# Optimization experiments

Hardware: AMD Instinct MI355X
Metric: run time of the kernel (lower is better)

## Reference

```python
import jax, jax.numpy as jnp
import numpy as np

EPS = 1e-5  # instance-norm epsilon (NormalizeLayer over spatial axes)

def instance_norm(x):
    # normalize over spatial axes (1,2) per sample, per channel
    mean = jnp.mean(x, axis=(1, 2), keepdims=True)
    var = jnp.var(x, axis=(1, 2), keepdims=True)
    return (x - mean) / jnp.sqrt(var + EPS)

def l2norm(x, axis=-1):
    return x / jnp.sqrt(jnp.sum(x * x, axis=axis, keepdims=True) + 1e-12)

def setup_inputs() -> dict:
    key = jax.random.key(0)
    ks = jax.random.split(key, 5)
    B, H, W, C = 4, 64, 64, 256
    content = jax.random.normal(ks[0], (B, H, W, C), jnp.float32)
    style = jax.random.normal(ks[1], (B, H, W, C), jnp.float32)
    scale = 1.0 / np.sqrt(C)
    Wq = jax.random.normal(ks[2], (C, C), jnp.float32) * scale
    Wk = jax.random.normal(ks[3], (C, C), jnp.float32) * scale
    Wv = jax.random.normal(ks[4], (C, C), jnp.float32) * scale
    bq = jnp.zeros((C,), jnp.float32)
    bk = jnp.zeros((C,), jnp.float32)
    bv = jnp.zeros((C,), jnp.float32)
    return {"content": content, "style": style, "Wq": Wq, "bq": bq,
            "Wk": Wk, "bk": bk, "Wv": Wv, "bv": bv}

def reference(content, style, Wq, bq, Wk, bk, Wv, bv):
    B, H, W, C = content.shape
    N = H * W
    norm_content = instance_norm(content)
    norm_style = instance_norm(style)
    # 1x1 convs == per-pixel linear layers
    Q = (jnp.einsum('bhwc,cd->bhwd', norm_content, Wq) + bq).reshape(B, N, C)
    K = (jnp.einsum('bhwc,cd->bhwd', norm_style, Wk) + bk).reshape(B, N, C)
    V = (jnp.einsum('bhwc,cd->bhwd', style, Wv) + bv).reshape(B, N, C)
    # cosine-similarity attention (Dot with normalize=True)
    attn = jnp.einsum('bnc,bmc->bnm', l2norm(Q), l2norm(K))  # [B, N, N]
    A = jax.nn.softmax(attn, axis=-1)
    M = jnp.einsum('bnm,bmc->bnc', A, V)                 # weighted mean
    S2 = jnp.einsum('bnm,bmc->bnc', A, V * V) - M * M    # weighted variance
    S2 = jax.nn.relu(S2)
    # safe sqrt: grad-safe at exactly 0 (matches sqrt(relu(x)) values)
    S = jnp.where(S2 > 0, jnp.sqrt(jnp.where(S2 > 0, S2, 1.0)), 0.0)
    S = S.reshape(B, H, W, C)
    M = M.reshape(B, H, W, C)
    return S * norm_content + M
```

## Files before the change

### kernel.cpp

```cpp
#include <hip/hip_runtime.h>
#include <cstdint>

#define BB 4
#define NN 4096
#define CC 256

typedef __attribute__((ext_vector_type(8))) short bf16x8;
typedef __attribute__((ext_vector_type(4))) short bf16x4;
typedef __attribute__((ext_vector_type(4))) float f32x4;
typedef unsigned int u32;
typedef __attribute__((ext_vector_type(4))) u32 u32x4;

#define MFMA_BF16(a, b, c) __builtin_amdgcn_mfma_f32_16x16x32_bf16((a), (b), (c), 0, 0, 0)
#define MFMA_FP8(a, b, c)  __builtin_amdgcn_mfma_f32_16x16x32_fp8_fp8((a), (b), (c), 0, 0, 0)

#define WAITCNT(vm, xp, lgkm) (((vm) & 0xF) | (((vm) >> 4) << 14) | ((xp) << 4) | ((lgkm) << 8))

__device__ __forceinline__ unsigned short f2bf(float f) {
  union { float f; unsigned u; } v; v.f = f;
  unsigned r = v.u + 0x7fffu + ((v.u >> 16) & 1u);
  return (unsigned short)(r >> 16);
}
__device__ __forceinline__ float bf2f(unsigned short h) {
  union { unsigned u; float f; } v; v.u = ((unsigned)h) << 16;
  return v.f;
}
__device__ __forceinline__ u32 pk4_fp8(float a, float b, float c, float d) {
  u32 v = (u32)__builtin_amdgcn_cvt_pk_fp8_f32(a, b, 0, false);
  v = (u32)__builtin_amdgcn_cvt_pk_fp8_f32(c, d, (int)v, true);
  return v;
}

typedef __attribute__((address_space(3))) unsigned int lds_u32;
typedef __attribute__((address_space(1))) unsigned int glb_u32;

__device__ __forceinline__ void async_cp16(const void* g, void* l) {
  __builtin_amdgcn_global_load_lds((const glb_u32*)g,
                                   (lds_u32*)(unsigned)(unsigned long long)l,
                                   16, 0, 0);
}

__global__ __launch_bounds__(256) void transpose_w(const float* __restrict__ Wq,
                                                   const float* __restrict__ Wk,
                                                   const float* __restrict__ Wv,
                                                   unsigned short* __restrict__ Wt) {
  __shared__ float sT[64 * 65];
  int blk = blockIdx.x;
  int z = blk / 16, tl = blk % 16;
  int c0 = (tl >> 2) * 64, d0 = (tl & 3) * 64;
  const float* W = (z == 0) ? Wq : ((z == 1) ? Wk : Wv);
  #pragma unroll
  for (int i = 0; i < 16; ++i) {
    int e = i * 256 + threadIdx.x;
    int c = e >> 6, d = e & 63;
    sT[c * 65 + d] = W[(size_t)(c0 + c) * CC + d0 + d];
  }
  __syncthreads();
  #pragma unroll
  for (int i = 0; i < 16; ++i) {
    int e = i * 256 + threadIdx.x;
    int d = e >> 6, c = e & 63;
    Wt[(size_t)z * 65536 + (size_t)(d0 + d) * CC + c0 + c] = f2bf(sT[c * 65 + d]);
  }
}

__global__ __launch_bounds__(256) void stats_partial(const float* __restrict__ content,
                                                     const float* __restrict__ style,
                                                     float* __restrict__ sums) {
  int blk = blockIdx.x;
  int t = blk >> 9, b = (blk >> 7) & 3, chunk = blk & 127;
  const float* X = t ? style : content;
  int c = threadIdx.x;
  const float* base = X + ((size_t)b * NN + (size_t)chunk * 32) * CC + c;
  float s = 0.f, ss = 0.f;
  #pragma unroll 8
  for (int r = 0; r < 32; ++r) {
    float x = base[(size_t)r * CC];
    s += x; ss += x * x;
  }
  atomicAdd(&sums[((t * 2 + 0) * BB + b) * CC + c], s);
  atomicAdd(&sums[((t * 2 + 1) * BB + b) * CC + c], ss);
}

__global__ __launch_bounds__(256) void stats_finalize(const float* __restrict__ sums,
                                                      float* __restrict__ stats) {
  int i = blockIdx.x * 256 + threadIdx.x;
  int t = i >> 10, bc = i & 1023;
  float s = sums[(t * 2 + 0) * 1024 + bc];
  float ss = sums[(t * 2 + 1) * 1024 + bc];
  float m = s * (1.0f / NN);
  float var = ss * (1.0f / NN) - m * m;
  stats[(t * 2 + 0) * 1024 + bc] = m;
  stats[(t * 2 + 1) * 1024 + bc] = rsqrtf(var + 1e-5f);
}

__global__ __launch_bounds__(256, 2) void qkv_kernel(
    const float* __restrict__ content, const float* __restrict__ style,
    const unsigned short* __restrict__ Wt,
    const float* __restrict__ bq, const float* __restrict__ bk, const float* __restrict__ bv,
    const float* __restrict__ stats,
    unsigned char* __restrict__ Qn, unsigned char* __restrict__ Kn,
    unsigned char* __restrict__ Vct) {
  __shared__ unsigned short sX[64 * 256];
  __shared__ unsigned short sWOT[256 * 64];
  __shared__ float sSq[64];

  int tid = threadIdx.x;
  int wid = tid >> 6, lane = tid & 63, quad = lane >> 4, l16 = lane & 15;
  int uwid = __builtin_amdgcn_readfirstlane(wid);
  int tileid = blockIdx.x;
  int z = blockIdx.y;
  int gr0 = tileid * 64;
  int b = gr0 >> 12;

  const float* X = (z == 0) ? content : style;
  int statt = (z == 0) ? 0 : 1;
  const float* mean = stats + ((statt * 2 + 0) * BB + b) * CC;
  const float* rstd = stats + ((statt * 2 + 1) * BB + b) * CC;
  bool donorm = (z < 2);

  if (tid < 64) sSq[tid] = 0.f;

  {
    int row = tid >> 2;
    int c0 = (tid & 3) * 64;
    const float* xr = X + (size_t)(gr0 + row) * CC;
    #pragma unroll
    for (int i = 0; i < 8; ++i) {
      int c = c0 + i * 8;
      f32x4 xa = *(const f32x4*)(xr + c);
      f32x4 xb = *(const f32x4*)(xr + c + 4);
      float xv[8] = {xa.x, xa.y, xa.z, xa.w, xb.x, xb.y, xb.z, xb.w};
      bf16x8 hh;
      #pragma unroll
      for (int j = 0; j < 8; ++j) {
        float x = xv[j];
        if (donorm) x = (x - mean[c + j]) * rstd[c + j];
        hh[j] = (short)f2bf(x);
      }
      int jchunk = (tid & 3) * 8 + (i ^ (row & 7));
      *(bf16x8*)(sX + row * 256 + jchunk * 8) = hh;
    }
  }

  f32x4 zero4 = {0.f, 0.f, 0.f, 0.f};
  f32x4 acc[4][4];
  #pragma unroll
  for (int i = 0; i < 4; ++i)
    #pragma unroll
    for (int j = 0; j < 4; ++j) acc[i][j] = zero4;

  int n0 = wid * 64;
  const unsigned short* wb = Wt + (size_t)z * 65536;

  for (int chn = 0; chn < 4; ++chn) {
    int kk0 = chn * 64;
    __syncthreads();
    #pragma unroll
    for (int it = 0; it < 8; ++it) {
      int L = it * 256 + wid * 64 + lane;
      int d = L >> 3, s = L & 7;
      int j = s ^ (d & 7);
      async_cp16(wb + d * 256 + kk0 + j * 8,
                 (char*)sWOT + (size_t)(it * 256 + uwid * 64) * 16);
    }
    __syncthreads();
    #pragma unroll
    for (int ks = 0; ks < 2; ++ks) {
      bf16x8 a[4];
      #pragma unroll
      for (int mf = 0; mf < 4; ++mf) {
        int row = mf * 16 + l16;
        int j = chn * 8 + ((ks * 4 + quad) ^ (row & 7));
        a[mf] = *(const bf16x8*)(sX + row * 256 + j * 8);
      }
      #pragma unroll
      for (int nf = 0; nf < 4; ++nf) {
        int d = n0 + nf * 16 + l16;
        int j = (ks * 4 + quad) ^ (d & 7);
        bf16x8 bw = *(const bf16x8*)(sWOT + d * 64 + j * 8);
        #pragma unroll
        for (int mf = 0; mf < 4; ++mf) acc[mf][nf] = MFMA_BF16(a[mf], bw, acc[mf][nf]);
      }
    }
  }

  const float* bias = (z == 0) ? bq : ((z == 1) ? bk : bv);
  #pragma unroll
  for (int nf = 0; nf < 4; ++nf) {
    float bb_ = bias[n0 + nf * 16 + l16];
    #pragma unroll
    for (int mf = 0; mf < 4; ++mf) {
      acc[mf][nf].x += bb_; acc[mf][nf].y += bb_;
      acc[mf][nf].z += bb_; acc[mf][nf].w += bb_;
    }
  }

  if (z < 2) {
    #pragma unroll
    for (int mf = 0; mf < 4; ++mf) {
      f32x4 ss = zero4;
      #pragma unroll
      for (int nf = 0; nf < 4; ++nf) ss += acc[mf][nf] * acc[mf][nf];
      #pragma unroll
      for (int m = 1; m < 16; m <<= 1) {
        ss.x += __shfl_xor(ss.x, m, 64);
        ss.y += __shfl_xor(ss.y, m, 64);
        ss.z += __shfl_xor(ss.z, m, 64);
        ss.w += __shfl_xor(ss.w, m, 64);
      }
      if (l16 == 0) {
        int r0 = mf * 16 + quad * 4;
        atomicAdd(&sSq[r0 + 0], ss.x);
        atomicAdd(&sSq[r0 + 1], ss.y);
        atomicAdd(&sSq[r0 + 2], ss.z);
        atomicAdd(&sSq[r0 + 3], ss.w);
      }
    }
    __syncthreads();
    if (tid < 64) sSq[tid] = rsqrtf(sSq[tid] + 1e-12f);
    __syncthreads();
    unsigned char* O = (z == 0) ? Qn : Kn;
    #pragma unroll
    for (int mf = 0; mf < 4; ++mf) {
      int r0 = mf * 16 + quad * 4;
      float rn0 = sSq[r0], rn1 = sSq[r0 + 1], rn2 = sSq[r0 + 2], rn3 = sSq[r0 + 3];
      #pragma unroll
      for (int nf = 0; nf < 4; ++nf) {
        int col = n0 + nf * 16 + l16;
        u32 p01 = (u32)__builtin_amdgcn_cvt_pk_fp8_f32(acc[mf][nf].x * rn0, acc[mf][nf].y * rn1, 0, false);
        u32 p23 = (u32)__builtin_amdgcn_cvt_pk_fp8_f32(acc[mf][nf].z * rn2, acc[mf][nf].w * rn3, 0, false);
        O[(size_t)(gr0 + r0 + 0) * CC + col] = (unsigned char)(p01 & 0xff);
        O[(size_t)(gr0 + r0 + 1) * CC + col] = (unsigned char)((p01 >> 8) & 0xff);
        O[(size_t)(gr0 + r0 + 2) * CC + col] = (unsigned char)(p23 & 0xff);
        O[(size_t)(gr0 + r0 + 3) * CC + col] = (unsigned char)((p23 >> 8) & 0xff);
      }
    }
  } else {
    __syncthreads();
    #pragma unroll
    for (int mf = 0; mf < 4; ++mf) {
      int j0 = mf * 2 + (quad >> 1);
      int sub = (quad & 1) * 4;
      #pragma unroll
      for (int nf = 0; nf < 4; ++nf) {
        int col = n0 + nf * 16 + l16;
        bf16x4 pk;
        pk[0] = (short)f2bf(acc[mf][nf].x);
        pk[1] = (short)f2bf(acc[mf][nf].y);
        pk[2] = (short)f2bf(acc[mf][nf].z);
        pk[3] = (short)f2bf(acc[mf][nf].w);
        *(bf16x4*)(sWOT + col * 64 + (j0 ^ (col & 7)) * 8 + sub) = pk;
      }
    }
    __syncthreads();
    int n_in_b = gr0 & (NN - 1);
    unsigned char* vrow  = Vct + ((size_t)(b * 512 + tid)) * NN + n_in_b;
    unsigned char* v2row = Vct + ((size_t)(b * 512 + 256 + tid)) * NN + n_in_b;
    #pragma unroll
    for (int i = 0; i < 4; ++i) {
      float f[16];
      #pragma unroll
      for (int g = 0; g < 2; ++g) {
        bf16x8 hv = *(const bf16x8*)(sWOT + tid * 64 + ((i * 2 + g) ^ (tid & 7)) * 8);
        #pragma unroll
        for (int j = 0; j < 8; ++j) f[g * 8 + j] = bf2f((unsigned short)hv[j]);
      }
      u32x4 v1, v2;
      v1.x = pk4_fp8(f[0], f[1], f[2], f[3]);
      v1.y = pk4_fp8(f[4], f[5], f[6], f[7]);
      v1.z = pk4_fp8(f[8], f[9], f[10], f[11]);
      v1.w = pk4_fp8(f[12], f[13], f[14], f[15]);
      v2.x = pk4_fp8(f[0]*f[0], f[1]*f[1], f[2]*f[2], f[3]*f[3]);
      v2.y = pk4_fp8(f[4]*f[4], f[5]*f[5], f[6]*f[6], f[7]*f[7]);
      v2.z = pk4_fp8(f[8]*f[8], f[9]*f[9], f[10]*f[10], f[11]*f[11]);
      v2.w = pk4_fp8(f[12]*f[12], f[13]*f[13], f[14]*f[14], f[15]*f[15]);
      *(u32x4*)(vrow + i * 16) = v1;
      *(u32x4*)(v2row + i * 16) = v2;
    }
  }
}

__global__ __launch_bounds__(512, 2) void flash_kernel(
    const unsigned char* __restrict__ Qn,
    const unsigned char* __restrict__ Kn,
    const unsigned char* __restrict__ Vct,
    const float* __restrict__ content,
    const float* __restrict__ stats,
    float* __restrict__ out) {
  __shared__ __align__(16) char smem[32768 + 65536 + 4096 + 256];
  char* sKb = smem;
  char* sVb = smem + 32768;
  char* sP  = smem + 98304;
  float* sL = (float*)(smem + 102400);
  float* sE2 = (float*)smem;

  int tid = threadIdx.x;
  int wid = tid >> 6, lane = tid & 63, quad = lane >> 4, l16 = lane & 15;
  int uwid = __builtin_amdgcn_readfirstlane(wid);

  int id = blockIdx.x;
  int b = (id >> 1) & 3;
  int tile = ((id >> 3) << 1) | (id & 1);
  int q0 = tile * 64;

  int qh = (wid & 1) * 32;
  int kb0 = (wid >> 1) * 16;
  int cw = wid * 64;

  long qf[2][8];
  #pragma unroll
  for (int mf = 0; mf < 2; ++mf) {
    int row = q0 + qh + mf * 16 + l16;
    const unsigned char* base = Qn + (((size_t)b * NN + row) << 8);
    #pragma unroll
    for (int kf = 0; kf < 8; ++kf)
      qf[mf][kf] = *(const long*)(base + kf * 32 + quad * 8);
  }
  __builtin_amdgcn_s_waitcnt(WAITCNT(0, 7, 15));

  if (tid < 64) sL[tid] = 0.f;

  const unsigned char* kbp = Kn + (((size_t)b * NN) << 8);
  const unsigned char* vbp = Vct + ((size_t)b * 512) * NN;

  auto stageK = [&](int k0, int buf) {
    char* dst = sKb + buf * 16384;
    #pragma unroll
    for (int it = 0; it < 2; ++it) {
      int L = it * 512 + wid * 64 + lane;
      int ky = L >> 4, s = L & 15;
      int c16 = s ^ (ky & 15);
      async_cp16(kbp + (((size_t)(k0 + ky)) << 8) + c16 * 16,
                 dst + (size_t)(it * 512 + uwid * 64) * 16);
    }
  };
  auto stageV = [&](int k0, int buf) {
    char* dst = sVb + buf * 32768;
    #pragma unroll
    for (int it = 0; it < 4; ++it) {
      int L = it * 512 + wid * 64 + lane;
      int r128 = L >> 3, s8 = L & 7;
      int x = s8 ^ (r128 & 7);
      int ch = (r128 << 1) | (x >> 2);
      int k16 = x & 3;
      async_cp16(vbp + (size_t)ch * NN + k0 + k16 * 16,
                 dst + (size_t)(it * 512 + uwid * 64) * 16);
    }
  };

  f32x4 zero4 = {0.f, 0.f, 0.f, 0.f};
  f32x4 om[4][4];
  #pragma unroll
  for (int i = 0; i < 4; ++i)
    #pragma unroll
    for (int j = 0; j < 4; ++j) om[i][j] = zero4;
  float Lr[8];
  #pragma unroll
  for (int i = 0; i < 8; ++i) Lr[i] = 0.f;

  stageK(0, 0);  stageV(0, 0);
  stageK(64, 1); stageV(64, 1);

  int keyrow = (kb0 + l16) * 256;
  int key15 = l16;
  int khalf = (quad & 1) * 8;

  for (int kt = 0; kt < 64; ++kt) {
    __builtin_amdgcn_s_waitcnt(WAITCNT(6, 7, 15));
    __builtin_amdgcn_s_barrier();

    const char* sKc = sKb + (kt & 1) * 16384;
    f32x4 s0 = zero4, s1 = zero4;
    #pragma unroll
    for (int kf = 0; kf < 8; ++kf) {
      int slot = (kf * 2 + (quad >> 1)) ^ key15;
      long bk = *(const long*)(sKc + keyrow + slot * 16 + khalf);
      s0 = MFMA_FP8(qf[0][kf], bk, s0);
      s1 = MFMA_FP8(qf[1][kf], bk, s1);
    }
    #pragma unroll
    for (int mf = 0; mf < 2; ++mf) {
      f32x4 sv = mf ? s1 : s0;
      float p0 = __expf(sv.x), p1 = __expf(sv.y), p2 = __expf(sv.z), p3 = __expf(sv.w);
      Lr[mf * 4 + 0] += p0; Lr[mf * 4 + 1] += p1;
      Lr[mf * 4 + 2] += p2; Lr[mf * 4 + 3] += p3;
      u32 b01 = (u32)__builtin_amdgcn_cvt_pk_fp8_f32(p0, p1, 0, false);
      u32 b23 = (u32)__builtin_amdgcn_cvt_pk_fp8_f32(p2, p3, 0, false);
      int qbase = qh + mf * 16 + quad * 4;
      #pragma unroll
      for (int r = 0; r < 4; ++r) {
        int q = qbase + r;
        u32 byte = (r < 2) ? ((r == 0) ? (b01 & 0xff) : ((b01 >> 8) & 0xff))
                           : ((r == 2) ? (b23 & 0xff) : ((b23 >> 8) & 0xff));
        int addr = (q >> 1) * 128 + ((((q & 1) * 4 + (wid >> 1))) ^ ((q >> 1) & 7)) * 16 + l16;
        sP[addr] = (unsigned char)byte;
      }
    }
    __builtin_amdgcn_s_waitcnt(WAITCNT(63, 7, 0));
    __builtin_amdgcn_s_barrier();

    const char* sVc = sVb + (kt & 1) * 32768;
    long pf[2][4], vf[2][4];
    #pragma unroll
    for (int ks = 0; ks < 2; ++ks) {
      int c16 = ks * 2 + (quad >> 1);
      #pragma unroll
      for (int mf2 = 0; mf2 < 4; ++mf2) {
        int q = mf2 * 16 + l16;
        pf[ks][mf2] = *(const long*)(sP + (q >> 1) * 128 +
                        (((q & 1) * 4 + c16) ^ ((q >> 1) & 7)) * 16 + khalf);
      }
      #pragma unroll
      for (int nf = 0; nf < 4; ++nf) {
        int ch = cw + nf * 16 + l16;
        vf[ks][nf] = *(const long*)(sVc + (ch >> 1) * 128 +
                        (((ch & 1) * 4 + c16) ^ ((ch >> 1) & 7)) * 16 + khalf);
      }
    }
    __builtin_amdgcn_s_waitcnt(WAITCNT(63, 7, 0));
    __builtin_amdgcn_s_barrier();

    int nk = ((kt + 2) & 63) * 64;
    stageK(nk, kt & 1);
    stageV(nk, kt & 1);

    #pragma unroll
    for (int ks = 0; ks < 2; ++ks)
      #pragma unroll
      for (int nf = 0; nf < 4; ++nf)
        #pragma unroll
        for (int mf2 = 0; mf2 < 4; ++mf2)
          om[mf2][nf] = MFMA_FP8(pf[ks][mf2], vf[ks][nf], om[mf2][nf]);
  }

  #pragma unroll
  for (int i = 0; i < 8; ++i) {
    #pragma unroll
    for (int m = 1; m < 16; m <<= 1) Lr[i] += __shfl_xor(Lr[i], m, 64);
  }
  if (l16 == 0) {
    #pragma unroll
    for (int mf = 0; mf < 2; ++mf)
      #pragma unroll
      for (int r = 0; r < 4; ++r)
        atomicAdd(&sL[qh + mf * 16 + quad * 4 + r], Lr[mf * 4 + r]);
  }
  __builtin_amdgcn_s_waitcnt(WAITCNT(0, 7, 0));
  __builtin_amdgcn_s_barrier();

  if (wid >= 4) {
    #pragma unroll
    for (int mf2 = 0; mf2 < 4; ++mf2) {
      #pragma unroll
      for (int nf = 0; nf < 4; ++nf) {
        int ch = (wid - 4) * 64 + nf * 16 + l16;
        int cidx = (mf2 * 4 + quad) ^ (ch & 15);
        *(f32x4*)(sE2 + ch * 64 + cidx * 4) = om[mf2][nf];
      }
    }
  }
  __syncthreads();

  if (wid < 4) {
    const float* meanc = stats + (0 * BB + b) * CC;
    const float* rstdc = stats + (1 * BB + b) * CC;
    float linv[4][4];
    #pragma unroll
    for (int mf2 = 0; mf2 < 4; ++mf2)
      #pragma unroll
      for (int r = 0; r < 4; ++r)
        linv[mf2][r] = 1.0f / sL[mf2 * 16 + quad * 4 + r];
    #pragma unroll
    for (int nf = 0; nf < 4; ++nf) {
      int ch = cw + nf * 16 + l16;
      float mc = meanc[ch], rc = rstdc[ch];
      #pragma unroll
      for (int mf2 = 0; mf2 < 4; ++mf2) {
        int cidx = (mf2 * 4 + quad) ^ (ch & 15);
        f32x4 vv = *(const f32x4*)(sE2 + ch * 64 + cidx * 4);
        f32x4 ov = om[mf2][nf];
        #pragma unroll
        for (int r = 0; r < 4; ++r) {
          int row = mf2 * 16 + quad * 4 + r;
          float li = linv[mf2][r];
          float ovr = (r == 0) ? ov.x : (r == 1) ? ov.y : (r == 2) ? ov.z : ov.w;
          float vvr = (r == 0) ? vv.x : (r == 1) ? vv.y : (r == 2) ? vv.z : vv.w;
          float M = ovr * li;
          float E2 = vvr * li;
          float S2 = E2 - M * M;
          float S = (S2 > 0.f) ? sqrtf(S2) : 0.f;
          size_t gi = (((size_t)b * NN + q0 + row) << 8) + ch;
          float xh = (content[gi] - mc) * rc;
          out[gi] = S * xh + M;
        }
      }
    }
  }
}

extern "C" void kernel_launch(void* const* d_in, const int* in_sizes, int n_in,
                              void* d_out, int out_size, void* d_ws, size_t ws_size,
                              hipStream_t stream) {
  const float* content = (const float*)d_in[0];
  const float* style   = (const float*)d_in[1];
  const float* Wq = (const float*)d_in[2];
  const float* bq = (const float*)d_in[3];
  const float* Wk = (const float*)d_in[4];
  const float* bk = (const float*)d_in[5];
  const float* Wv = (const float*)d_in[6];
  const float* bv = (const float*)d_in[7];
  char* ws = (char*)d_ws;

  float* sums        = (float*)(ws + 0);
  float* stats       = (float*)(ws + 16384);
  unsigned short* Wt = (unsigned short*)(ws + 32768);
  unsigned char* Qn  = (unsigned char*)(ws + 425984);
  unsigned char* Kn  = (unsigned char*)(ws + 4620288);
  unsigned char* Vct = (unsigned char*)(ws + 8814592);
  float* outp = (float*)d_out;

  hipMemsetAsync(d_ws, 0, 16384, stream);
  hipLaunchKernelGGL(transpose_w, dim3(48), dim3(256), 0, stream, Wq, Wk, Wv, Wt);
  hipLaunchKernelGGL(stats_partial, dim3(1024), dim3(256), 0, stream, content, style, sums);
  hipLaunchKernelGGL(stats_finalize, dim3(8), dim3(256), 0, stream, sums, stats);
  hipLaunchKernelGGL(qkv_kernel, dim3(256, 3), dim3(256), 0, stream,
                     content, style, Wt, bq, bk, bv, stats, Qn, Kn, Vct);
  hipLaunchKernelGGL(flash_kernel, dim3(256), dim3(512), 0, stream,
                     Qn, Kn, Vct, content, stats, outp);
}
```

Before: 249.4 us.

## Restructure flash kernel to 32-query tiles with 256-thread blocks

Halves the query tile per block (32 rows) and the block size (4 waves), doubling the grid to 512 blocks. Each wave now computes scores for its own 16-key slice with K as the A operand and writes P as packed 32-bit words into a double-buffered P tile. V is single-buffered and staged one tile ahead, with V fragments loaded before the barrier, which removes one barrier per iteration. The aim is better CU occupancy and less LDS per block, at the cost of twice the K/V traffic per query, since each block streams all keys for fewer queries.

```diff
diff --git a/kernel.cpp b/kernel.cpp
--- a/kernel.cpp
+++ b/kernel.cpp
@@ -281,18 +281,20 @@
   }
 }
 
-__global__ __launch_bounds__(512, 2) void flash_kernel(
+__global__ __launch_bounds__(256, 2) void flash_kernel(
     const unsigned char* __restrict__ Qn,
     const unsigned char* __restrict__ Kn,
     const unsigned char* __restrict__ Vct,
     const float* __restrict__ content,
     const float* __restrict__ stats,
     float* __restrict__ out) {
-  __shared__ __align__(16) char smem[32768 + 65536 + 4096 + 256];
+  __shared__ __align__(16) char smem[32768 + 32768 + 4096 + 128];
   char* sKb = smem;
-  char* sVb = smem + 32768;
-  char* sP  = smem + 98304;
-  float* sL = (float*)(smem + 102400);
+  char* sVb = smem + 65536;
+  char* sPb = smem + 32768;
+  sVb = smem + 36864;
+  sPb = smem + 32768;
+  float* sL = (float*)(smem + 69632);
   float* sE2 = (float*)smem;
 
   int tid = threadIdx.x;
@@ -302,24 +304,19 @@
   int id = blockIdx.x;
   int b = (id >> 1) & 3;
   int tile = ((id >> 3) << 1) | (id & 1);
-  int q0 = tile * 64;
-
-  int qh = (wid & 1) * 32;
-  int kb0 = (wid >> 1) * 16;
-  int cw = wid * 64;
+  int q0 = tile * 32;
 
   long qf[2][8];
   #pragma unroll
-  for (int mf = 0; mf < 2; ++mf) {
-    int row = q0 + qh + mf * 16 + l16;
-    const unsigned char* base = Qn + (((size_t)b * NN + row) << 8);
+  for (int ng = 0; ng < 2; ++ng) {
+    const unsigned char* base = Qn + (((size_t)b * NN + q0 + ng * 16 + l16) << 8);
     #pragma unroll
     for (int kf = 0; kf < 8; ++kf)
-      qf[mf][kf] = *(const long*)(base + kf * 32 + quad * 8);
+      qf[ng][kf] = *(const long*)(base + kf * 32 + quad * 8);
   }
   __builtin_amdgcn_s_waitcnt(WAITCNT(0, 7, 15));
 
-  if (tid < 64) sL[tid] = 0.f;
+  if (tid < 32) sL[tid] = 0.f;
 
   const unsigned char* kbp = Kn + (((size_t)b * NN) << 8);
   const unsigned char* vbp = Vct + ((size_t)b * 512) * NN;
@@ -327,163 +324,143 @@
   auto stageK = [&](int k0, int buf) {
     char* dst = sKb + buf * 16384;
     #pragma unroll
-    for (int it = 0; it < 2; ++it) {
-      int L = it * 512 + wid * 64 + lane;
-      int ky = L >> 4, s = L & 15;
-      int c16 = s ^ (ky & 15);
+    for (int it = 0; it < 4; ++it) {
+      int L = it * 256 + wid * 64 + lane;
+      int ky = L >> 4;
+      int c16 = (L & 15) ^ (ky & 15);
       async_cp16(kbp + (((size_t)(k0 + ky)) << 8) + c16 * 16,
-                 dst + (size_t)(it * 512 + uwid * 64) * 16);
+                 dst + (size_t)(it * 256 + uwid * 64) * 16);
     }
   };
-  auto stageV = [&](int k0, int buf) {
-    char* dst = sVb + buf * 32768;
-    #pragma unroll
-    for (int it = 0; it < 4; ++it) {
-      int L = it * 512 + wid * 64 + lane;
-      int r128 = L >> 3, s8 = L & 7;
-      int x = s8 ^ (r128 & 7);
-      int ch = (r128 << 1) | (x >> 2);
-      int k16 = x & 3;
-      async_cp16(vbp + (size_t)ch * NN + k0 + k16 * 16,
-                 dst + (size_t)(it * 512 + uwid * 64) * 16);
+  auto stageV = [&](int k0) {
+    #pragma unroll
+    for (int it = 0; it < 8; ++it) {
+      int L = it * 256 + wid * 64 + lane;
+      int ch = L >> 2;
+      int c16 = (L & 3) ^ ((ch >> 1) & 3);
+      async_cp16(vbp + (size_t)ch * NN + k0 + c16 * 16,
+                 sVb + (size_t)(it * 256 + uwid * 64) * 16);
     }
   };
 
   f32x4 zero4 = {0.f, 0.f, 0.f, 0.f};
-  f32x4 om[4][4];
-  #pragma unroll
-  for (int i = 0; i < 4; ++i)
-    #pragma unroll
-    for (int j = 0; j < 4; ++j) om[i][j] = zero4;
-  float Lr[8];
-  #pragma unroll
-  for (int i = 0; i < 8; ++i) Lr[i] = 0.f;
-
-  stageK(0, 0);  stageV(0, 0);
-  stageK(64, 1); stageV(64, 1);
-
-  int keyrow = (kb0 + l16) * 256;
-  int key15 = l16;
-  int khalf = (quad & 1) * 8;
+  f32x4 om[2][8];
+  #pragma unroll
+  for (int i = 0; i < 2; ++i)
+    #pragma unroll
+    for (int j = 0; j < 8; ++j) om[i][j] = zero4;
+  float Lr[2] = {0.f, 0.f};
+
+  stageK(0, 0);
+  stageV(0);
+  stageK(64, 1);
+
+  int cwch[2];
+  (void)cwch;
 
   for (int kt = 0; kt < 64; ++kt) {
-    __builtin_amdgcn_s_waitcnt(WAITCNT(6, 7, 15));
+    __builtin_amdgcn_s_waitcnt(WAITCNT(4, 7, 15));
     __builtin_amdgcn_s_barrier();
 
     const char* sKc = sKb + (kt & 1) * 16384;
+    char* sPc = sPb + (kt & 1) * 2048;
+
     f32x4 s0 = zero4, s1 = zero4;
     #pragma unroll
     for (int kf = 0; kf < 8; ++kf) {
-      int slot = (kf * 2 + (quad >> 1)) ^ key15;
-      long bk = *(const long*)(sKc + keyrow + slot * 16 + khalf);
-      s0 = MFMA_FP8(qf[0][kf], bk, s0);
-      s1 = MFMA_FP8(qf[1][kf], bk, s1);
-    }
-    #pragma unroll
-    for (int mf = 0; mf < 2; ++mf) {
-      f32x4 sv = mf ? s1 : s0;
+      long ak = *(const long*)(sKc + (wid * 16 + l16) * 256 +
+                               ((kf * 2 + (quad >> 1)) ^ l16) * 16 + (quad & 1) * 8);
+      s0 = MFMA_FP8(ak, qf[0][kf], s0);
+      s1 = MFMA_FP8(ak, qf[1][kf], s1);
+    }
+    #pragma unroll
+    for (int ng = 0; ng < 2; ++ng) {
+      f32x4 sv = ng ? s1 : s0;
       float p0 = __expf(sv.x), p1 = __expf(sv.y), p2 = __expf(sv.z), p3 = __expf(sv.w);
-      Lr[mf * 4 + 0] += p0; Lr[mf * 4 + 1] += p1;
-      Lr[mf * 4 + 2] += p2; Lr[mf * 4 + 3] += p3;
-      u32 b01 = (u32)__builtin_amdgcn_cvt_pk_fp8_f32(p0, p1, 0, false);
-      u32 b23 = (u32)__builtin_amdgcn_cvt_pk_fp8_f32(p2, p3, 0, false);
-      int qbase = qh + mf * 16 + quad * 4;
-      #pragma unroll
-      for (int r = 0; r < 4; ++r) {
-        int q = qbase + r;
-        u32 byte = (r < 2) ? ((r == 0) ? (b01 & 0xff) : ((b01 >> 8) & 0xff))
-                           : ((r == 2) ? (b23 & 0xff) : ((b23 >> 8) & 0xff));
-        int addr = (q >> 1) * 128 + ((((q & 1) * 4 + (wid >> 1))) ^ ((q >> 1) & 7)) * 16 + l16;
-        sP[addr] = (unsigned char)byte;
-      }
-    }
+      Lr[ng] += p0 + p1 + p2 + p3;
+      u32 w = pk4_fp8(p0, p1, p2, p3);
+      int q = ng * 16 + l16;
+      int chunk8 = wid * 2 + (quad >> 1);
+      *(u32*)(sPc + q * 64 + ((chunk8 ^ (q & 7)) * 8) + (quad & 1) * 4) = w;
+    }
+    long vf[2][8];
+    #pragma unroll
+    for (int ks = 0; ks < 2; ++ks)
+      #pragma unroll
+      for (int cg = 0; cg < 8; ++cg) {
+        int ch = wid * 128 + cg * 16 + l16;
+        int slot = (ks * 2 + (quad >> 1)) ^ ((ch >> 1) & 3);
+        vf[ks][cg] = *(const long*)(sVb + ch * 64 + slot * 16 + (quad & 1) * 8);
+      }
     __builtin_amdgcn_s_waitcnt(WAITCNT(63, 7, 0));
     __builtin_amdgcn_s_barrier();
 
-    const char* sVc = sVb + (kt & 1) * 32768;
-    long pf[2][4], vf[2][4];
-    #pragma unroll
-    for (int ks = 0; ks < 2; ++ks) {
-      int c16 = ks * 2 + (quad >> 1);
-      #pragma unroll
-      for (int mf2 = 0; mf2 < 4; ++mf2) {
-        int q = mf2 * 16 + l16;
-        pf[ks][mf2] = *(const long*)(sP + (q >> 1) * 128 +
-                        (((q & 1) * 4 + c16) ^ ((q >> 1) & 7)) * 16 + khalf);
-      }
-      #pragma unroll
-      for (int nf = 0; nf < 4; ++nf) {
-        int ch = cw + nf * 16 + l16;
-        vf[ks][nf] = *(const long*)(sVc + (ch >> 1) * 128 +
-                        (((ch & 1) * 4 + c16) ^ ((ch >> 1) & 7)) * 16 + khalf);
-      }
-    }
-    __builtin_amdgcn_s_waitcnt(WAITCNT(63, 7, 0));
-    __builtin_amdgcn_s_barrier();
-
-    int nk = ((kt + 2) & 63) * 64;
-    stageK(nk, kt & 1);
-    stageV(nk, kt & 1);
-
+    stageV(((kt + 1) & 63) * 64);
+    stageK(((kt + 2) & 63) * 64, kt & 1);
+
+    long pf[2][2];
     #pragma unroll
     for (int ks = 0; ks < 2; ++ks)
       #pragma unroll
-      for (int nf = 0; nf < 4; ++nf)
+      for (int mq = 0; mq < 2; ++mq) {
+        int q = mq * 16 + l16;
+        pf[ks][mq] = *(const long*)(sPc + q * 64 + (((ks * 4 + quad) ^ (q & 7)) * 8));
+      }
+    #pragma unroll
+    for (int ks = 0; ks < 2; ++ks)
+      #pragma unroll
+      for (int cg = 0; cg < 8; ++cg)
         #pragma unroll
-        for (int mf2 = 0; mf2 < 4; ++mf2)
-          om[mf2][nf] = MFMA_FP8(pf[ks][mf2], vf[ks][nf], om[mf2][nf]);
-  }
-
-  #pragma unroll
-  for (int i = 0; i < 8; ++i) {
-    #pragma unroll
-    for (int m = 1; m < 16; m <<= 1) Lr[i] += __shfl_xor(Lr[i], m, 64);
-  }
-  if (l16 == 0) {
-    #pragma unroll
-    for (int mf = 0; mf < 2; ++mf)
-      #pragma unroll
-      for (int r = 0; r < 4; ++r)
-        atomicAdd(&sL[qh + mf * 16 + quad * 4 + r], Lr[mf * 4 + r]);
+        for (int mq = 0; mq < 2; ++mq)
+          om[mq][cg] = MFMA_FP8(pf[ks][mq], vf[ks][cg], om[mq][cg]);
+  }
+
+  #pragma unroll
+  for (int ng = 0; ng < 2; ++ng) {
+    Lr[ng] += __shfl_xor(Lr[ng], 16, 64);
+    Lr[ng] += __shfl_xor(Lr[ng], 32, 64);
+  }
+  if (quad == 0) {
+    atomicAdd(&sL[l16], Lr[0]);
+    atomicAdd(&sL[16 + l16], Lr[1]);
   }
   __builtin_amdgcn_s_waitcnt(WAITCNT(0, 7, 0));
   __builtin_amdgcn_s_barrier();
 
-  if (wid >= 4) {
-    #pragma unroll
-    for (int mf2 = 0; mf2 < 4; ++mf2) {
-      #pragma unroll
-      for (int nf = 0; nf < 4; ++nf) {
-        int ch = (wid - 4) * 64 + nf * 16 + l16;
-        int cidx = (mf2 * 4 + quad) ^ (ch & 15);
-        *(f32x4*)(sE2 + ch * 64 + cidx * 4) = om[mf2][nf];
-      }
-    }
+  if (wid >= 2) {
+    #pragma unroll
+    for (int mq = 0; mq < 2; ++mq)
+      #pragma unroll
+      for (int cg = 0; cg < 8; ++cg) {
+        int ch = (wid - 2) * 128 + cg * 16 + l16;
+        int c4 = (mq * 4 + quad) ^ (ch & 7);
+        *(f32x4*)(sE2 + ch * 32 + c4 * 4) = om[mq][cg];
+      }
   }
   __syncthreads();
 
-  if (wid < 4) {
+  if (wid < 2) {
     const float* meanc = stats + (0 * BB + b) * CC;
     const float* rstdc = stats + (1 * BB + b) * CC;
-    float linv[4][4];
-    #pragma unroll
-    for (int mf2 = 0; mf2 < 4; ++mf2)
+    float linv[2][4];
+    #pragma unroll
+    for (int mq = 0; mq < 2; ++mq)
       #pragma unroll
       for (int r = 0; r < 4; ++r)
-        linv[mf2][r] = 1.0f / sL[mf2 * 16 + quad * 4 + r];
-    #pragma unroll
-    for (int nf = 0; nf < 4; ++nf) {
-      int ch = cw + nf * 16 + l16;
+        linv[mq][r] = 1.0f / sL[mq * 16 + quad * 4 + r];
+    #pragma unroll
+    for (int cg = 0; cg < 8; ++cg) {
+      int ch = wid * 128 + cg * 16 + l16;
       float mc = meanc[ch], rc = rstdc[ch];
       #pragma unroll
-      for (int mf2 = 0; mf2 < 4; ++mf2) {
-        int cidx = (mf2 * 4 + quad) ^ (ch & 15);
-        f32x4 vv = *(const f32x4*)(sE2 + ch * 64 + cidx * 4);
-        f32x4 ov = om[mf2][nf];
+      for (int mq = 0; mq < 2; ++mq) {
+        int c4 = (mq * 4 + quad) ^ (ch & 7);
+        f32x4 vv = *(const f32x4*)(sE2 + ch * 32 + c4 * 4);
+        f32x4 ov = om[mq][cg];
         #pragma unroll
         for (int r = 0; r < 4; ++r) {
-          int row = mf2 * 16 + quad * 4 + r;
-          float li = linv[mf2][r];
+          int row = mq * 16 + quad * 4 + r;
+          float li = linv[mq][r];
           float ovr = (r == 0) ? ov.x : (r == 1) ? ov.y : (r == 2) ? ov.z : ov.w;
           float vvr = (r == 0) ? vv.x : (r == 1) ? vv.y : (r == 2) ? vv.z : vv.w;
           float M = ovr * li;
@@ -526,6 +503,6 @@
   hipLaunchKernelGGL(stats_finalize, dim3(8), dim3(256), 0, stream, sums, stats);
   hipLaunchKernelGGL(qkv_kernel, dim3(256, 3), dim3(256), 0, stream,
                      content, style, Wt, bq, bk, bv, stats, Qn, Kn, Vct);
-  hipLaunchKernelGGL(flash_kernel, dim3(256), dim3(512), 0, stream,
+  hipLaunchKernelGGL(flash_kernel, dim3(512), dim3(256), 0, stream,
                      Qn, Kn, Vct, content, stats, outp);
 }
```

Result: slower. 255.8 us (+2.6%).

## Switch QKV projection to FP8 MFMA with 128-row tiles and per-wave row norms

Applied to the files above, without the earlier changes.

The QKV projection kernel now stores the weights and normalized inputs as FP8 instead of BF16 and uses FP8 MFMA. Each block handles 128 rows, with each wave owning 32 full rows across all 256 output columns. Because a wave holds whole rows, the L2 row norm is finished with shuffles alone, removing the shared-memory atomics and two barriers. The V/V² transpose now stages FP8 directly in two passes. This halves weight and input staging traffic and MFMA work, but adds FP8 quantization error to the projection inputs and uses more accumulator registers per thread.

```diff
diff --git a/kernel.cpp b/kernel.cpp
--- a/kernel.cpp
+++ b/kernel.cpp
@@ -11,7 +11,6 @@
 typedef unsigned int u32;
 typedef __attribute__((ext_vector_type(4))) u32 u32x4;
 
-#define MFMA_BF16(a, b, c) __builtin_amdgcn_mfma_f32_16x16x32_bf16((a), (b), (c), 0, 0, 0)
 #define MFMA_FP8(a, b, c)  __builtin_amdgcn_mfma_f32_16x16x32_fp8_fp8((a), (b), (c), 0, 0, 0)
 
 #define WAITCNT(vm, xp, lgkm) (((vm) & 0xF) | (((vm) >> 4) << 14) | ((xp) << 4) | ((lgkm) << 8))
@@ -21,15 +20,14 @@
   unsigned r = v.u + 0x7fffu + ((v.u >> 16) & 1u);
   return (unsigned short)(r >> 16);
 }
-__device__ __forceinline__ float bf2f(unsigned short h) {
-  union { unsigned u; float f; } v; v.u = ((unsigned)h) << 16;
-  return v.f;
-}
 __device__ __forceinline__ u32 pk4_fp8(float a, float b, float c, float d) {
   u32 v = (u32)__builtin_amdgcn_cvt_pk_fp8_f32(a, b, 0, false);
   v = (u32)__builtin_amdgcn_cvt_pk_fp8_f32(c, d, (int)v, true);
   return v;
 }
+__device__ __forceinline__ unsigned char fp8_1(float a) {
+  return (unsigned char)(((u32)__builtin_amdgcn_cvt_pk_fp8_f32(a, a, 0, false)) & 0xff);
+}
 
 typedef __attribute__((address_space(3))) unsigned int lds_u32;
 typedef __attribute__((address_space(1))) unsigned int glb_u32;
@@ -43,7 +41,7 @@
 __global__ __launch_bounds__(256) void transpose_w(const float* __restrict__ Wq,
                                                    const float* __restrict__ Wk,
                                                    const float* __restrict__ Wv,
-                                                   unsigned short* __restrict__ Wt) {
+                                                   unsigned char* __restrict__ Wt8) {
   __shared__ float sT[64 * 65];
   int blk = blockIdx.x;
   int z = blk / 16, tl = blk % 16;
@@ -60,7 +58,7 @@
   for (int i = 0; i < 16; ++i) {
     int e = i * 256 + threadIdx.x;
     int d = e >> 6, c = e & 63;
-    Wt[(size_t)z * 65536 + (size_t)(d0 + d) * CC + c0 + c] = f2bf(sT[c * 65 + d]);
+    Wt8[(size_t)z * 65536 + (size_t)(d0 + d) * CC + c0 + c] = fp8_1(sT[c * 65 + d]);
   }
 }
 
@@ -96,21 +94,20 @@
 
 __global__ __launch_bounds__(256, 2) void qkv_kernel(
     const float* __restrict__ content, const float* __restrict__ style,
-    const unsigned short* __restrict__ Wt,
+    const unsigned char* __restrict__ Wt8,
     const float* __restrict__ bq, const float* __restrict__ bk, const float* __restrict__ bv,
     const float* __restrict__ stats,
     unsigned char* __restrict__ Qn, unsigned char* __restrict__ Kn,
     unsigned char* __restrict__ Vct) {
-  __shared__ unsigned short sX[64 * 256];
-  __shared__ unsigned short sWOT[256 * 64];
-  __shared__ float sSq[64];
+  __shared__ __align__(16) char sW[32768];
+  __shared__ __align__(16) char sX[32768];
 
   int tid = threadIdx.x;
   int wid = tid >> 6, lane = tid & 63, quad = lane >> 4, l16 = lane & 15;
   int uwid = __builtin_amdgcn_readfirstlane(wid);
   int tileid = blockIdx.x;
   int z = blockIdx.y;
-  int gr0 = tileid * 64;
+  int gr0 = tileid * 128;
   int b = gr0 >> 12;
 
   const float* X = (z == 0) ? content : style;
@@ -119,89 +116,93 @@
   const float* rstd = stats + ((statt * 2 + 1) * BB + b) * CC;
   bool donorm = (z < 2);
 
-  if (tid < 64) sSq[tid] = 0.f;
-
-  {
-    int row = tid >> 2;
-    int c0 = (tid & 3) * 64;
-    const float* xr = X + (size_t)(gr0 + row) * CC;
-    #pragma unroll
-    for (int i = 0; i < 8; ++i) {
-      int c = c0 + i * 8;
-      f32x4 xa = *(const f32x4*)(xr + c);
-      f32x4 xb = *(const f32x4*)(xr + c + 4);
-      float xv[8] = {xa.x, xa.y, xa.z, xa.w, xb.x, xb.y, xb.z, xb.w};
-      bf16x8 hh;
-      #pragma unroll
-      for (int j = 0; j < 8; ++j) {
-        float x = xv[j];
-        if (donorm) x = (x - mean[c + j]) * rstd[c + j];
-        hh[j] = (short)f2bf(x);
-      }
-      int jchunk = (tid & 3) * 8 + (i ^ (row & 7));
-      *(bf16x8*)(sX + row * 256 + jchunk * 8) = hh;
-    }
+  #pragma unroll
+  for (int i = 0; i < 8; ++i) {
+    int lin = i * 256 + tid;
+    int row = lin >> 4, c16 = lin & 15;
+    int c = c16 * 16;
+    const float* xr = X + (size_t)(gr0 + row) * CC + c;
+    f32x4 x0 = *(const f32x4*)(xr + 0);
+    f32x4 x1 = *(const f32x4*)(xr + 4);
+    f32x4 x2 = *(const f32x4*)(xr + 8);
+    f32x4 x3 = *(const f32x4*)(xr + 12);
+    if (donorm) {
+      f32x4 m0 = *(const f32x4*)(mean + c + 0), r0 = *(const f32x4*)(rstd + c + 0);
+      f32x4 m1 = *(const f32x4*)(mean + c + 4), r1 = *(const f32x4*)(rstd + c + 4);
+      f32x4 m2 = *(const f32x4*)(mean + c + 8), r2 = *(const f32x4*)(rstd + c + 8);
+      f32x4 m3 = *(const f32x4*)(mean + c + 12), r3 = *(const f32x4*)(rstd + c + 12);
+      x0 = (x0 - m0) * r0; x1 = (x1 - m1) * r1;
+      x2 = (x2 - m2) * r2; x3 = (x3 - m3) * r3;
+    }
+    u32x4 pk;
+    pk.x = pk4_fp8(x0.x, x0.y, x0.z, x0.w);
+    pk.y = pk4_fp8(x1.x, x1.y, x1.z, x1.w);
+    pk.z = pk4_fp8(x2.x, x2.y, x2.z, x2.w);
+    pk.w = pk4_fp8(x3.x, x3.y, x3.z, x3.w);
+    *(u32x4*)(sX + row * 256 + ((c16 ^ (row & 15)) * 16)) = pk;
   }
 
   f32x4 zero4 = {0.f, 0.f, 0.f, 0.f};
-  f32x4 acc[4][4];
-  #pragma unroll
-  for (int i = 0; i < 4; ++i)
-    #pragma unroll
-    for (int j = 0; j < 4; ++j) acc[i][j] = zero4;
-
-  int n0 = wid * 64;
-  const unsigned short* wb = Wt + (size_t)z * 65536;
-
-  for (int chn = 0; chn < 4; ++chn) {
-    int kk0 = chn * 64;
+  f32x4 acc[2][16];
+  #pragma unroll
+  for (int i = 0; i < 2; ++i)
+    #pragma unroll
+    for (int j = 0; j < 16; ++j) acc[i][j] = zero4;
+
+  const unsigned char* wb = Wt8 + (size_t)z * 65536;
+
+  for (int half = 0; half < 2; ++half) {
     __syncthreads();
     #pragma unroll
     for (int it = 0; it < 8; ++it) {
       int L = it * 256 + wid * 64 + lane;
-      int d = L >> 3, s = L & 7;
-      int j = s ^ (d & 7);
-      async_cp16(wb + d * 256 + kk0 + j * 8,
-                 (char*)sWOT + (size_t)(it * 256 + uwid * 64) * 16);
+      int d = L >> 3;
+      int c16 = (L & 7) ^ (d & 7);
+      async_cp16(wb + (size_t)d * 256 + half * 128 + c16 * 16,
+                 sW + (size_t)(it * 256 + uwid * 64) * 16);
     }
     __syncthreads();
-    #pragma unroll
-    for (int ks = 0; ks < 2; ++ks) {
-      bf16x8 a[4];
-      #pragma unroll
-      for (int mf = 0; mf < 4; ++mf) {
-        int row = mf * 16 + l16;
-        int j = chn * 8 + ((ks * 4 + quad) ^ (row & 7));
-        a[mf] = *(const bf16x8*)(sX + row * 256 + j * 8);
-      }
-      #pragma unroll
-      for (int nf = 0; nf < 4; ++nf) {
-        int d = n0 + nf * 16 + l16;
-        int j = (ks * 4 + quad) ^ (d & 7);
-        bf16x8 bw = *(const bf16x8*)(sWOT + d * 64 + j * 8);
-        #pragma unroll
-        for (int mf = 0; mf < 4; ++mf) acc[mf][nf] = MFMA_BF16(a[mf], bw, acc[mf][nf]);
+
+    long a[2][4];
+    #pragma unroll
+    for (int mf = 0; mf < 2; ++mf) {
+      int row = wid * 32 + mf * 16 + l16;
+      #pragma unroll
+      for (int kc = 0; kc < 4; ++kc) {
+        int chunk = half * 8 + kc * 2 + (quad >> 1);
+        a[mf][kc] = *(const long*)(sX + row * 256 + ((chunk ^ (row & 15)) * 16) + (quad & 1) * 8);
+      }
+    }
+    #pragma unroll
+    for (int nf = 0; nf < 16; ++nf) {
+      int d = nf * 16 + l16;
+      #pragma unroll
+      for (int kc = 0; kc < 4; ++kc) {
+        long bw = *(const long*)(sW + d * 128 + (((kc * 2 + (quad >> 1)) ^ (d & 7)) * 16) + (quad & 1) * 8);
+        acc[0][nf] = MFMA_FP8(a[0][kc], bw, acc[0][nf]);
+        acc[1][nf] = MFMA_FP8(a[1][kc], bw, acc[1][nf]);
       }
     }
   }
 
   const float* bias = (z == 0) ? bq : ((z == 1) ? bk : bv);
   #pragma unroll
-  for (int nf = 0; nf < 4; ++nf) {
-    float bb_ = bias[n0 + nf * 16 + l16];
-    #pragma unroll
-    for (int mf = 0; mf < 4; ++mf) {
+  for (int nf = 0; nf < 16; ++nf) {
+    float bb_ = bias[nf * 16 + l16];
+    #pragma unroll
+    for (int mf = 0; mf < 2; ++mf) {
       acc[mf][nf].x += bb_; acc[mf][nf].y += bb_;
       acc[mf][nf].z += bb_; acc[mf][nf].w += bb_;
     }
   }
 
   if (z < 2) {
-    #pragma unroll
-    for (int mf = 0; mf < 4; ++mf) {
+    unsigned char* O = (z == 0) ? Qn : Kn;
+    #pragma unroll
+    for (int mf = 0; mf < 2; ++mf) {
       f32x4 ss = zero4;
       #pragma unroll
-      for (int nf = 0; nf < 4; ++nf) ss += acc[mf][nf] * acc[mf][nf];
+      for (int nf = 0; nf < 16; ++nf) ss += acc[mf][nf] * acc[mf][nf];
       #pragma unroll
       for (int m = 1; m < 16; m <<= 1) {
         ss.x += __shfl_xor(ss.x, m, 64);
@@ -209,27 +210,15 @@
         ss.z += __shfl_xor(ss.z, m, 64);
         ss.w += __shfl_xor(ss.w, m, 64);
       }
-      if (l16 == 0) {
-        int r0 = mf * 16 + quad * 4;
-        atomicAdd(&sSq[r0 + 0], ss.x);
-        atomicAdd(&sSq[r0 + 1], ss.y);
-        atomicAdd(&sSq[r0 + 2], ss.z);
-        atomicAdd(&sSq[r0 + 3], ss.w);
-      }
-    }
-    __syncthreads();
-    if (tid < 64) sSq[tid] = rsqrtf(sSq[tid] + 1e-12f);
-    __syncthreads();
-    unsigned char* O = (z == 0) ? Qn : Kn;
-    #pragma unroll
-    for (int mf = 0; mf < 4; ++mf) {
-      int r0 = mf * 16 + quad * 4;
-      float rn0 = sSq[r0], rn1 = sSq[r0 + 1], rn2 = sSq[r0 + 2], rn3 = sSq[r0 + 3];
-      #pragma unroll
-      for (int nf = 0; nf < 4; ++nf) {
-        int col = n0 + nf * 16 + l16;
-        u32 p01 = (u32)__builtin_amdgcn_cvt_pk_fp8_f32(acc[mf][nf].x * rn0, acc[mf][nf].y * rn1, 0, false);
-        u32 p23 = (u32)__builtin_amdgcn_cvt_pk_fp8_f32(acc[mf][nf].z * rn2, acc[mf][nf].w * rn3, 0, false);
+      f32x4 rq;
+      rq.x = rsqrtf(ss.x + 1e-12f); rq.y = rsqrtf(ss.y + 1e-12f);
+      rq.z = rsqrtf(ss.z + 1e-12f); rq.w = rsqrtf(ss.w + 1e-12f);
+      int r0 = wid * 32 + mf * 16 + quad * 4;
+      #pragma unroll
+      for (int nf = 0; nf < 16; ++nf) {
+        int col = nf * 16 + l16;
+        u32 p01 = (u32)__builtin_amdgcn_cvt_pk_fp8_f32(acc[mf][nf].x * rq.x, acc[mf][nf].y * rq.y, 0, false);
+        u32 p23 = (u32)__builtin_amdgcn_cvt_pk_fp8_f32(acc[mf][nf].z * rq.z, acc[mf][nf].w * rq.w, 0, false);
         O[(size_t)(gr0 + r0 + 0) * CC + col] = (unsigned char)(p01 & 0xff);
         O[(size_t)(gr0 + r0 + 1) * CC + col] = (unsigned char)((p01 >> 8) & 0xff);
         O[(size_t)(gr0 + r0 + 2) * CC + col] = (unsigned char)(p23 & 0xff);
@@ -237,46 +226,33 @@
       }
     }
   } else {
+    char* sOT = sX;
+    int n_in_b = gr0 & (NN - 1);
     __syncthreads();
     #pragma unroll
-    for (int mf = 0; mf < 4; ++mf) {
-      int j0 = mf * 2 + (quad >> 1);
-      int sub = (quad & 1) * 4;
-      #pragma unroll
-      for (int nf = 0; nf < 4; ++nf) {
-        int col = n0 + nf * 16 + l16;
-        bf16x4 pk;
-        pk[0] = (short)f2bf(acc[mf][nf].x);
-        pk[1] = (short)f2bf(acc[mf][nf].y);
-        pk[2] = (short)f2bf(acc[mf][nf].z);
-        pk[3] = (short)f2bf(acc[mf][nf].w);
-        *(bf16x4*)(sWOT + col * 64 + (j0 ^ (col & 7)) * 8 + sub) = pk;
-      }
-    }
-    __syncthreads();
-    int n_in_b = gr0 & (NN - 1);
-    unsigned char* vrow  = Vct + ((size_t)(b * 512 + tid)) * NN + n_in_b;
-    unsigned char* v2row = Vct + ((size_t)(b * 512 + 256 + tid)) * NN + n_in_b;
-    #pragma unroll
-    for (int i = 0; i < 4; ++i) {
-      float f[16];
-      #pragma unroll
-      for (int g = 0; g < 2; ++g) {
-        bf16x8 hv = *(const bf16x8*)(sWOT + tid * 64 + ((i * 2 + g) ^ (tid & 7)) * 8);
+    for (int pass = 0; pass < 2; ++pass) {
+      #pragma unroll
+      for (int mf = 0; mf < 2; ++mf) {
+        int j = wid * 2 + mf;
+        int r4 = wid * 32 + mf * 16 + quad * 4;
+        (void)r4;
         #pragma unroll
-        for (int j = 0; j < 8; ++j) f[g * 8 + j] = bf2f((unsigned short)hv[j]);
-      }
-      u32x4 v1, v2;
-      v1.x = pk4_fp8(f[0], f[1], f[2], f[3]);
-      v1.y = pk4_fp8(f[4], f[5], f[6], f[7]);
-      v1.z = pk4_fp8(f[8], f[9], f[10], f[11]);
-      v1.w = pk4_fp8(f[12], f[13], f[14], f[15]);
-      v2.x = pk4_fp8(f[0]*f[0], f[1]*f[1], f[2]*f[2], f[3]*f[3]);
-      v2.y = pk4_fp8(f[4]*f[4], f[5]*f[5], f[6]*f[6], f[7]*f[7]);
-      v2.z = pk4_fp8(f[8]*f[8], f[9]*f[9], f[10]*f[10], f[11]*f[11]);
-      v2.w = pk4_fp8(f[12]*f[12], f[13]*f[13], f[14]*f[14], f[15]*f[15]);
-      *(u32x4*)(vrow + i * 16) = v1;
-      *(u32x4*)(v2row + i * 16) = v2;
+        for (int nf = 0; nf < 16; ++nf) {
+          int col = nf * 16 + l16;
+          f32x4 v = acc[mf][nf];
+          f32x4 w = pass ? (v * v) : v;
+          u32 pk = pk4_fp8(w.x, w.y, w.z, w.w);
+          *(u32*)(sOT + col * 128 + ((j ^ (col & 7)) * 16) + quad * 4) = pk;
+        }
+      }
+      __syncthreads();
+      unsigned char* orow = Vct + ((size_t)(b * 512 + (pass ? 256 : 0) + tid)) * NN + n_in_b;
+      #pragma unroll
+      for (int j = 0; j < 8; ++j) {
+        u32x4 val = *(const u32x4*)(sOT + tid * 128 + ((j ^ (tid & 7)) * 16));
+        *(u32x4*)(orow + j * 16) = val;
+      }
+      __syncthreads();
     }
   }
 }
@@ -514,18 +490,18 @@
 
   float* sums        = (float*)(ws + 0);
   float* stats       = (float*)(ws + 16384);
-  unsigned short* Wt = (unsigned short*)(ws + 32768);
-  unsigned char* Qn  = (unsigned char*)(ws + 425984);
-  unsigned char* Kn  = (unsigned char*)(ws + 4620288);
-  unsigned char* Vct = (unsigned char*)(ws + 8814592);
+  unsigned char* Wt8 = (unsigned char*)(ws + 32768);
+  unsigned char* Qn  = (unsigned char*)(ws + 229376);
+  unsigned char* Kn  = (unsigned char*)(ws + 4423680);
+  unsigned char* Vct = (unsigned char*)(ws + 8617984);
   float* outp = (float*)d_out;
 
   hipMemsetAsync(d_ws, 0, 16384, stream);
-  hipLaunchKernelGGL(transpose_w, dim3(48), dim3(256), 0, stream, Wq, Wk, Wv, Wt);
+  hipLaunchKernelGGL(transpose_w, dim3(48), dim3(256), 0, stream, Wq, Wk, Wv, Wt8);
   hipLaunchKernelGGL(stats_partial, dim3(1024), dim3(256), 0, stream, content, style, sums);
   hipLaunchKernelGGL(stats_finalize, dim3(8), dim3(256), 0, stream, sums, stats);
-  hipLaunchKernelGGL(qkv_kernel, dim3(256, 3), dim3(256), 0, stream,
-                     content, style, Wt, bq, bk, bv, stats, Qn, Kn, Vct);
+  hipLaunchKernelGGL(qkv_kernel, dim3(128, 3), dim3(256), 0, stream,
+                     content, style, Wt8, bq, bk, bv, stats, Qn, Kn, Vct);
   hipLaunchKernelGGL(flash_kernel, dim3(256), dim3(512), 0, stream,
                      Qn, Kn, Vct, content, stats, outp);
 }
```

Result: faster. 233.5 us (-6.4%).
